# Kernel optimization log

Hardware: AMD Instinct MI355X
Metric: run time of the kernel (lower is better)

## Reference

```python
import jax, jax.numpy as jnp
import numpy as np

T, B, IN, H, OUT = 128, 128, 512, 512, 512


def _lstm_dir(x, W_ih, W_hh, b_ih, b_hh):
    # x: [T, B, IN]; W_ih: [4H, IN]; W_hh: [4H, H]; biases: [4H]
    # Precompute input contribution for all timesteps in one big GEMM.
    xw = jnp.einsum('tbi,gi->tbg', x, W_ih) + b_ih + b_hh  # [T, B, 4H]
    Hh = W_hh.shape[1]

    def step(carry, xw_t):
        h, c = carry
        gates = xw_t + h @ W_hh.T  # [B, 4H]
        i, f, g, o = jnp.split(gates, 4, axis=-1)  # PyTorch gate order i,f,g,o
        i = jax.nn.sigmoid(i)
        f = jax.nn.sigmoid(f)
        g = jnp.tanh(g)
        o = jax.nn.sigmoid(o)
        c = f * c + i * g
        h = o * jnp.tanh(c)
        return (h, c), h

    h0 = jnp.zeros((x.shape[1], Hh), x.dtype)
    c0 = jnp.zeros((x.shape[1], Hh), x.dtype)
    _, hs = jax.lax.scan(step, (h0, c0), xw)
    return hs  # [T, B, H]


def setup_inputs() -> dict:
    key = jax.random.key(0)
    ks = jax.random.split(key, 12)
    s_in = 1.0 / np.sqrt(H)
    u = lambda k, shape: jax.random.uniform(k, shape, jnp.float32, -s_in, s_in)
    return {
        'x': jax.random.normal(ks[0], (T, B, IN), jnp.float32),
        'W_ih_f': u(ks[1], (4 * H, IN)),
        'W_hh_f': u(ks[2], (4 * H, H)),
        'b_ih_f': u(ks[3], (4 * H,)),
        'b_hh_f': u(ks[4], (4 * H,)),
        'W_ih_b': u(ks[5], (4 * H, IN)),
        'W_hh_b': u(ks[6], (4 * H, H)),
        'b_ih_b': u(ks[7], (4 * H,)),
        'b_hh_b': u(ks[8], (4 * H,)),
        'W_lin': u(ks[9], (OUT, 2 * H)),
        'b_lin': u(ks[10], (OUT,)),
    }


def reference(x, W_ih_f, W_hh_f, b_ih_f, b_hh_f, W_ih_b, W_hh_b, b_ih_b, b_hh_b, W_lin, b_lin):
    h_fwd = _lstm_dir(x, W_ih_f, W_hh_f, b_ih_f, b_hh_f)                    # [T,B,H]
    h_bwd = _lstm_dir(x[::-1], W_ih_b, W_hh_b, b_ih_b, b_hh_b)[::-1]        # [T,B,H]
    out = jnp.concatenate([h_fwd, h_bwd], axis=-1)                          # [T,B,2H]
    out = jnp.einsum('tbh,oh->tbo', out, W_lin) + b_lin                     # [T,B,OUT]
    return out
```

## Files before the change

### kernel.cpp

```cpp
#include <hip/hip_runtime.h>

typedef unsigned short u16;
typedef unsigned long long u64;
typedef __attribute__((ext_vector_type(8))) short bf16x8;
typedef __attribute__((ext_vector_type(4))) float f32x4;

#define MFMA16(a, b, c) __builtin_amdgcn_mfma_f32_16x16x32_bf16((a), (b), (c), 0, 0, 0)

#define TT 128
#define BB 128
#define IN_ 512
#define HH 512
#define G4 2048
#define OUTD 512
#define TB 16384

__device__ __forceinline__ u16 f2bf(float f) {
    union { float f; unsigned u; } v; v.f = f;
    unsigned r = v.u + 0x7FFFu + ((v.u >> 16) & 1u);
    return (u16)(r >> 16);
}
__device__ __forceinline__ float bf2f(u16 h) {
    union { unsigned u; float f; } v; v.u = ((unsigned)h) << 16; return v.f;
}
__device__ __forceinline__ float sigmoid_f(float x) { return 1.f / (1.f + __expf(-x)); }
__device__ __forceinline__ float tanh_f(float x) {
    float e = __expf(2.f * x);
    return 1.f - 2.f / (e + 1.f);
}

__global__ void cvt_kernel(const float* __restrict__ src, u16* __restrict__ dst, int n4) {
    int i = blockIdx.x * blockDim.x + threadIdx.x;
    int stride = gridDim.x * blockDim.x;
    for (; i < n4; i += stride) {
        float4 v = ((const float4*)src)[i];
        ushort4 o;
        o.x = f2bf(v.x); o.y = f2bf(v.y); o.z = f2bf(v.z); o.w = f2bf(v.w);
        ((ushort4*)dst)[i] = o;
    }
}

__global__ void bias_kernel(const float* __restrict__ bihf, const float* __restrict__ bhhf,
                            float* __restrict__ bf_, const float* __restrict__ bihb,
                            const float* __restrict__ bhhb, float* __restrict__ bb_, int n) {
    int i = blockIdx.x * blockDim.x + threadIdx.x;
    if (i < n) {
        bf_[i] = bihf[i] + bhhf[i];
        bb_[i] = bihb[i] + bhhb[i];
    }
}

__global__ void zero_exch_kernel(uint4* __restrict__ p) {
    int i = blockIdx.x * blockDim.x + threadIdx.x;
    p[i] = uint4{0u, 0u, 0u, 0u};
}

__global__ __launch_bounds__(256) void gemm_bias_kernel(
    const u16* __restrict__ A, const u16* __restrict__ W,
    const float* __restrict__ bias, void* __restrict__ Cout,
    int M, int N, int K, int out_is_bf16) {
    __shared__ __align__(16) u16 lA[128 * 72];
    __shared__ __align__(16) u16 lB[128 * 72];
    const int tid = threadIdx.x;
    const int m0 = blockIdx.x * 128;
    const int n0 = blockIdx.y * 128;
    const int wave = tid >> 6, lane = tid & 63;
    const int wm = wave >> 1, wn = wave & 1;
    const int lrow = lane & 15, lq = lane >> 4;

    f32x4 acc[4][4] = {};

    for (int kc = 0; kc < K; kc += 64) {
        #pragma unroll
        for (int i = 0; i < 4; ++i) {
            int c = i * 256 + tid;
            int row = c >> 3, off = c & 7;
            *(uint4*)(&lA[row * 72 + off * 8]) =
                *(const uint4*)(&A[(size_t)(m0 + row) * K + kc + off * 8]);
            *(uint4*)(&lB[row * 72 + off * 8]) =
                *(const uint4*)(&W[(size_t)(n0 + row) * K + kc + off * 8]);
        }
        __syncthreads();
        #pragma unroll
        for (int ks = 0; ks < 2; ++ks) {
            bf16x8 af[4], bfr[4];
            #pragma unroll
            for (int mf = 0; mf < 4; ++mf)
                af[mf] = *(const bf16x8*)(&lA[(wm * 64 + mf * 16 + lrow) * 72 + ks * 32 + lq * 8]);
            #pragma unroll
            for (int nf = 0; nf < 4; ++nf)
                bfr[nf] = *(const bf16x8*)(&lB[(wn * 64 + nf * 16 + lrow) * 72 + ks * 32 + lq * 8]);
            #pragma unroll
            for (int mf = 0; mf < 4; ++mf)
                #pragma unroll
                for (int nf = 0; nf < 4; ++nf)
                    acc[mf][nf] = MFMA16(af[mf], bfr[nf], acc[mf][nf]);
        }
        __syncthreads();
    }

    #pragma unroll
    for (int mf = 0; mf < 4; ++mf) {
        #pragma unroll
        for (int nf = 0; nf < 4; ++nf) {
            int row = m0 + wm * 64 + mf * 16 + lq * 4;
            int col = n0 + wn * 64 + nf * 16 + lrow;
            float bv = bias[col];
            f32x4 v = acc[mf][nf];
            #pragma unroll
            for (int r = 0; r < 4; ++r) {
                float val = v[r] + bv;
                if (out_is_bf16)
                    ((u16*)Cout)[(size_t)(row + r) * N + col] = f2bf(val);
                else
                    ((float*)Cout)[(size_t)(row + r) * N + col] = val;
            }
        }
    }
}

__global__ __launch_bounds__(256, 1) void lstm_persist_kernel(
    const u16* __restrict__ xw_f, const u16* __restrict__ xw_b,
    const u16* __restrict__ whh_f, const u16* __restrict__ whh_b,
    u16* __restrict__ hcat, u64* __restrict__ exch) {
    const int bx = blockIdx.x;
    const int dir = bx >> 7;
    const int bt = (bx >> 4) & 7;
    const int jt = bx & 15;
    const u16* __restrict__ xw  = dir ? xw_b : xw_f;
    const u16* __restrict__ whh = dir ? whh_b : whh_f;
    const int b0 = bt * 16;
    const int j0 = jt * 32;

    __shared__ __align__(16) u16 lh[16 * 520];
    __shared__ float sgate[4][16][33];

    const int tid = threadIdx.x;
    const int wave = tid >> 6, lane = tid & 63;
    const int lrow = lane & 15, lq = lane >> 4;

    const u16* wrow = whh + ((size_t)wave * HH + j0) * HH;
    bf16x8 w0[16], w1[16];
    #pragma unroll
    for (int kc = 0; kc < 16; ++kc) {
        w0[kc] = *(const bf16x8*)(&wrow[(size_t)lrow * HH + kc * 32 + lq * 8]);
        w1[kc] = *(const bf16x8*)(&wrow[(size_t)(16 + lrow) * HH + kc * 32 + lq * 8]);
    }
    #pragma unroll
    for (int kc = 0; kc < 16; ++kc)
        asm volatile("" : "+v"(w0[kc]), "+v"(w1[kc]));

    const int bl = tid >> 4;
    const int jj = (tid & 15) * 2;
    float cr0 = 0.f, cr1 = 0.f;

    const size_t my_ex = ((size_t)(dir)*BB + b0 + bl) * 256 + (j0 >> 1) + (tid & 15);

    for (int s = 0; s < TT; ++s) {
        const int t = dir ? (TT - 1 - s) : s;

        const u16* xrow = xw + ((size_t)t * BB + b0 + bl) * G4 + j0 + jj;
        unsigned xg[4];
        #pragma unroll
        for (int g = 0; g < 4; ++g)
            xg[g] = *(const unsigned*)(xrow + (size_t)g * HH);

        f32x4 acc0 = {}, acc1 = {}, acc0b = {}, acc1b = {};
        if (s > 0) {
            const int p = (s - 1) & 1;
            const u64* ex = exch + ((size_t)(p * 2 + dir) * BB + b0) * 256 + tid;
            const u64 expect = ((u64)(unsigned)s << 48) | ((u64)(unsigned)s << 16);
            u64 v[16];
            for (;;) {
                #pragma unroll
                for (int i = 0; i < 16; ++i)
                    v[i] = __hip_atomic_load(ex + (size_t)i * 256,
                                             __ATOMIC_RELAXED, __HIP_MEMORY_SCOPE_AGENT);
                bool ok = true;
                #pragma unroll
                for (int i = 0; i < 16; ++i)
                    ok &= ((v[i] & 0xFFFF0000FFFF0000ull) == expect);
                if (ok) break;
            }
            #pragma unroll
            for (int i = 0; i < 16; ++i)
                *(unsigned*)(&lh[i * 520 + tid * 2]) =
                    (unsigned)(v[i] & 0xffffu) | (unsigned)((v[i] >> 16) & 0xffff0000u);
            __syncthreads();

            #pragma unroll
            for (int kc = 0; kc < 16; kc += 2) {
                bf16x8 a0 = *(const bf16x8*)(&lh[lrow * 520 + kc * 32 + lq * 8]);
                bf16x8 a1 = *(const bf16x8*)(&lh[lrow * 520 + (kc + 1) * 32 + lq * 8]);
                acc0  = MFMA16(a0, w0[kc], acc0);
                acc1  = MFMA16(a0, w1[kc], acc1);
                acc0b = MFMA16(a1, w0[kc + 1], acc0b);
                acc1b = MFMA16(a1, w1[kc + 1], acc1b);
            }
            acc0 += acc0b;
            acc1 += acc1b;
        }

        #pragma unroll
        for (int r = 0; r < 4; ++r) {
            sgate[wave][lq * 4 + r][lrow]      = acc0[r];
            sgate[wave][lq * 4 + r][16 + lrow] = acc1[r];
        }
        __syncthreads();

        float gi0 = sgate[0][bl][jj]     + bf2f((u16)(xg[0] & 0xffffu));
        float gf0 = sgate[1][bl][jj]     + bf2f((u16)(xg[1] & 0xffffu));
        float gg0 = sgate[2][bl][jj]     + bf2f((u16)(xg[2] & 0xffffu));
        float go0 = sgate[3][bl][jj]     + bf2f((u16)(xg[3] & 0xffffu));
        float gi1 = sgate[0][bl][jj + 1] + bf2f((u16)(xg[0] >> 16));
        float gf1 = sgate[1][bl][jj + 1] + bf2f((u16)(xg[1] >> 16));
        float gg1 = sgate[2][bl][jj + 1] + bf2f((u16)(xg[2] >> 16));
        float go1 = sgate[3][bl][jj + 1] + bf2f((u16)(xg[3] >> 16));

        float c0 = sigmoid_f(gf0) * cr0 + sigmoid_f(gi0) * tanh_f(gg0);
        float c1 = sigmoid_f(gf1) * cr1 + sigmoid_f(gi1) * tanh_f(gg1);
        cr0 = c0; cr1 = c1;
        float h0 = sigmoid_f(go0) * tanh_f(c0);
        float h1 = sigmoid_f(go1) * tanh_f(c1);

        unsigned hb0 = (unsigned)f2bf(h0), hb1 = (unsigned)f2bf(h1);
        unsigned tagv = (unsigned)(s + 1) << 16;
        u64 pv = (u64)(tagv | hb0) | ((u64)(tagv | hb1) << 32);
        __hip_atomic_store(exch + (size_t)((s & 1) * 2) * BB * 256 + my_ex, pv,
                           __ATOMIC_RELAXED, __HIP_MEMORY_SCOPE_AGENT);

        *(unsigned*)(hcat + ((size_t)t * BB + b0 + bl) * (2 * HH) + dir * HH + j0 + jj) =
            hb0 | (hb1 << 16);
    }
}

#define OFF_XBF    ((size_t)0)
#define OFF_WIHF   (OFF_XBF  + (size_t)TB * IN_ * 2)
#define OFF_WIHB   (OFF_WIHF + (size_t)G4 * IN_ * 2)
#define OFF_WHHF   (OFF_WIHB + (size_t)G4 * IN_ * 2)
#define OFF_WHHB   (OFF_WHHF + (size_t)G4 * HH * 2)
#define OFF_WLIN   (OFF_WHHB + (size_t)G4 * HH * 2)
#define OFF_BIASF  (OFF_WLIN + (size_t)OUTD * 2 * HH * 2)
#define OFF_BIASB  (OFF_BIASF + (size_t)G4 * 4)
#define OFF_XWF    (OFF_BIASB + (size_t)G4 * 4)
#define OFF_XWB    (OFF_XWF  + (size_t)TB * G4 * 2)
#define OFF_HCAT   (OFF_XWB  + (size_t)TB * G4 * 2)
#define OFF_EXCH   (OFF_HCAT + (size_t)TB * 2 * HH * 2)
#define WS_NEED    (OFF_EXCH + (size_t)2 * 2 * BB * HH * 4)

extern "C" void kernel_launch(void* const* d_in, const int* in_sizes, int n_in,
                              void* d_out, int out_size, void* d_ws, size_t ws_size,
                              hipStream_t stream) {
    (void)in_sizes; (void)n_in; (void)out_size;
    if (ws_size < WS_NEED) return;

    const float* x    = (const float*)d_in[0];
    const float* Wihf = (const float*)d_in[1];
    const float* Whhf = (const float*)d_in[2];
    const float* bihf = (const float*)d_in[3];
    const float* bhhf = (const float*)d_in[4];
    const float* Wihb = (const float*)d_in[5];
    const float* Whhb = (const float*)d_in[6];
    const float* bihb = (const float*)d_in[7];
    const float* bhhb = (const float*)d_in[8];
    const float* Wlin = (const float*)d_in[9];
    const float* blin = (const float*)d_in[10];
    float* out = (float*)d_out;

    char* ws = (char*)d_ws;
    u16* x_bf    = (u16*)(ws + OFF_XBF);
    u16* wihf_bf = (u16*)(ws + OFF_WIHF);
    u16* wihb_bf = (u16*)(ws + OFF_WIHB);
    u16* whhf_bf = (u16*)(ws + OFF_WHHF);
    u16* whhb_bf = (u16*)(ws + OFF_WHHB);
    u16* wlin_bf = (u16*)(ws + OFF_WLIN);
    float* bias_f = (float*)(ws + OFF_BIASF);
    float* bias_b = (float*)(ws + OFF_BIASB);
    u16* xw_f = (u16*)(ws + OFF_XWF);
    u16* xw_b = (u16*)(ws + OFF_XWB);
    u16* hcat = (u16*)(ws + OFF_HCAT);
    u64* exch = (u64*)(ws + OFF_EXCH);

    cvt_kernel<<<2048, 256, 0, stream>>>(x, x_bf, (TB * IN_) / 4);
    cvt_kernel<<<512, 256, 0, stream>>>(Wihf, wihf_bf, (G4 * IN_) / 4);
    cvt_kernel<<<512, 256, 0, stream>>>(Wihb, wihb_bf, (G4 * IN_) / 4);
    cvt_kernel<<<512, 256, 0, stream>>>(Whhf, whhf_bf, (G4 * HH) / 4);
    cvt_kernel<<<512, 256, 0, stream>>>(Whhb, whhb_bf, (G4 * HH) / 4);
    cvt_kernel<<<512, 256, 0, stream>>>(Wlin, wlin_bf, (OUTD * 2 * HH) / 4);
    bias_kernel<<<8, 256, 0, stream>>>(bihf, bhhf, bias_f, bihb, bhhb, bias_b, G4);
    zero_exch_kernel<<<256, 256, 0, stream>>>((uint4*)exch);

    gemm_bias_kernel<<<dim3(TB / 128, G4 / 128), 256, 0, stream>>>(
        x_bf, wihf_bf, bias_f, xw_f, TB, G4, IN_, 1);
    gemm_bias_kernel<<<dim3(TB / 128, G4 / 128), 256, 0, stream>>>(
        x_bf, wihb_bf, bias_b, xw_b, TB, G4, IN_, 1);

    {
        void* args[] = { (void*)&xw_f, (void*)&xw_b, (void*)&whhf_bf, (void*)&whhb_bf,
                         (void*)&hcat, (void*)&exch };
        hipError_t e = hipLaunchCooperativeKernel(
            (const void*)lstm_persist_kernel, dim3(256), dim3(256), args, 0, stream);
        if (e != hipSuccess) {
            lstm_persist_kernel<<<256, 256, 0, stream>>>(xw_f, xw_b, whhf_bf, whhb_bf,
                                                         hcat, exch);
        }
    }

    gemm_bias_kernel<<<dim3(TB / 128, OUTD / 128), 256, 0, stream>>>(
        hcat, wlin_bf, blin, out, TB, OUTD, 2 * HH, 0);
}
```

Baseline: 698.1 us.

## Split recurrent GEMM over K across waves and feed MFMA directly from exchange loads

Each wave now owns a quarter of the hidden-state K dimension for all four gates, rather than one gate over the full K. Each lane loads its MFMA A-operand straight from the global exchange buffer, polls per chunk and strips tags in registers. This removes the LDS staging of h and one barrier, and lets MFMAs start on chunks that have already arrived. In exchange it needs a cross-wave reduction of partial sums through a larger shared buffer, and it adds an extra barrier before that buffer is written.

```diff
diff --git a/kernel.cpp b/kernel.cpp
--- a/kernel.cpp
+++ b/kernel.cpp
@@ -15,6 +15,8 @@
 #define OUTD 512
 #define TB 16384
 
+#define AEXLD(p) __hip_atomic_load((p), __ATOMIC_RELAXED, __HIP_MEMORY_SCOPE_AGENT)
+
 __device__ __forceinline__ u16 f2bf(float f) {
     union { float f; unsigned u; } v; v.f = f;
     unsigned r = v.u + 0x7FFFu + ((v.u >> 16) & 1u);
@@ -27,6 +29,9 @@
 __device__ __forceinline__ float tanh_f(float x) {
     float e = __expf(2.f * x);
     return 1.f - 2.f / (e + 1.f);
+}
+__device__ __forceinline__ unsigned striptag(u64 v) {
+    return (unsigned)(v & 0xffffu) | ((unsigned)(v >> 16) & 0xffff0000u);
 }
 
 __global__ void cvt_kernel(const float* __restrict__ src, u16* __restrict__ dst, int n4) {
@@ -132,29 +137,39 @@
     const int b0 = bt * 16;
     const int j0 = jt * 32;
 
-    __shared__ __align__(16) u16 lh[16 * 520];
-    __shared__ float sgate[4][16][33];
+    __shared__ float sg[4][4][16][33];
 
     const int tid = threadIdx.x;
     const int wave = tid >> 6, lane = tid & 63;
     const int lrow = lane & 15, lq = lane >> 4;
 
-    const u16* wrow = whh + ((size_t)wave * HH + j0) * HH;
-    bf16x8 w0[16], w1[16];
+    bf16x8 wreg[4][2][4];
     #pragma unroll
-    for (int kc = 0; kc < 16; ++kc) {
-        w0[kc] = *(const bf16x8*)(&wrow[(size_t)lrow * HH + kc * 32 + lq * 8]);
-        w1[kc] = *(const bf16x8*)(&wrow[(size_t)(16 + lrow) * HH + kc * 32 + lq * 8]);
-    }
+    for (int g = 0; g < 4; ++g)
+        #pragma unroll
+        for (int jh = 0; jh < 2; ++jh)
+            #pragma unroll
+            for (int ci = 0; ci < 4; ++ci)
+                wreg[g][jh][ci] = *(const bf16x8*)
+                    (&whh[(size_t)(g * HH + j0 + jh * 16 + lrow) * HH +
+                          (wave + ci * 4) * 32 + lq * 8]);
     #pragma unroll
-    for (int kc = 0; kc < 16; ++kc)
-        asm volatile("" : "+v"(w0[kc]), "+v"(w1[kc]));
+    for (int g = 0; g < 4; ++g)
+        #pragma unroll
+        for (int jh = 0; jh < 2; ++jh)
+            #pragma unroll
+            for (int ci = 0; ci < 4; ++ci)
+                asm volatile("" : "+v"(wreg[g][jh][ci]));
 
     const int bl = tid >> 4;
     const int jj = (tid & 15) * 2;
     float cr0 = 0.f, cr1 = 0.f;
 
-    const size_t my_ex = ((size_t)(dir)*BB + b0 + bl) * 256 + (j0 >> 1) + (tid & 15);
+    const size_t my_ex = ((size_t)dir * BB + b0 + bl) * 256 + (j0 >> 1) + (tid & 15);
+    const u64* exb0 = exch + ((size_t)(0 * 2 + dir) * BB + b0 + lrow) * 256 + lq * 4;
+    const u64* exb1 = exch + ((size_t)(1 * 2 + dir) * BB + b0 + lrow) * 256 + lq * 4;
+
+    const u64 TMASK = 0xFFFF0000FFFF0000ull;
 
     for (int s = 0; s < TT; ++s) {
         const int t = dir ? (TT - 1 - s) : s;
@@ -165,63 +180,70 @@
         for (int g = 0; g < 4; ++g)
             xg[g] = *(const unsigned*)(xrow + (size_t)g * HH);
 
-        f32x4 acc0 = {}, acc1 = {}, acc0b = {}, acc1b = {};
+        f32x4 acc[4][2] = {};
         if (s > 0) {
-            const int p = (s - 1) & 1;
-            const u64* ex = exch + ((size_t)(p * 2 + dir) * BB + b0) * 256 + tid;
+            const u64* eb = ((s - 1) & 1) ? exb1 : exb0;
             const u64 expect = ((u64)(unsigned)s << 48) | ((u64)(unsigned)s << 16);
-            u64 v[16];
-            for (;;) {
-                #pragma unroll
-                for (int i = 0; i < 16; ++i)
-                    v[i] = __hip_atomic_load(ex + (size_t)i * 256,
-                                             __ATOMIC_RELAXED, __HIP_MEMORY_SCOPE_AGENT);
-                bool ok = true;
-                #pragma unroll
-                for (int i = 0; i < 16; ++i)
-                    ok &= ((v[i] & 0xFFFF0000FFFF0000ull) == expect);
-                if (ok) break;
+
+            u64 v[4][4];
+            #pragma unroll
+            for (int ci = 0; ci < 4; ++ci) {
+                const u64* cp = eb + (size_t)(wave + ci * 4) * 16;
+                #pragma unroll
+                for (int k = 0; k < 4; ++k)
+                    v[ci][k] = AEXLD(cp + k);
             }
             #pragma unroll
-            for (int i = 0; i < 16; ++i)
-                *(unsigned*)(&lh[i * 520 + tid * 2]) =
-                    (unsigned)(v[i] & 0xffffu) | (unsigned)((v[i] >> 16) & 0xffff0000u);
-            __syncthreads();
-
-            #pragma unroll
-            for (int kc = 0; kc < 16; kc += 2) {
-                bf16x8 a0 = *(const bf16x8*)(&lh[lrow * 520 + kc * 32 + lq * 8]);
-                bf16x8 a1 = *(const bf16x8*)(&lh[lrow * 520 + (kc + 1) * 32 + lq * 8]);
-                acc0  = MFMA16(a0, w0[kc], acc0);
-                acc1  = MFMA16(a0, w1[kc], acc1);
-                acc0b = MFMA16(a1, w0[kc + 1], acc0b);
-                acc1b = MFMA16(a1, w1[kc + 1], acc1b);
+            for (int ci = 0; ci < 4; ++ci) {
+                const u64* cp = eb + (size_t)(wave + ci * 4) * 16;
+                for (;;) {
+                    bool ok = ((v[ci][0] & TMASK) == expect) &
+                              ((v[ci][1] & TMASK) == expect) &
+                              ((v[ci][2] & TMASK) == expect) &
+                              ((v[ci][3] & TMASK) == expect);
+                    if (ok) break;
+                    #pragma unroll
+                    for (int k = 0; k < 4; ++k)
+                        v[ci][k] = AEXLD(cp + k);
+                }
+                union { unsigned u[4]; bf16x8 b8; } ua;
+                #pragma unroll
+                for (int k = 0; k < 4; ++k)
+                    ua.u[k] = striptag(v[ci][k]);
+                bf16x8 a = ua.b8;
+                #pragma unroll
+                for (int g = 0; g < 4; ++g) {
+                    acc[g][0] = MFMA16(a, wreg[g][0][ci], acc[g][0]);
+                    acc[g][1] = MFMA16(a, wreg[g][1][ci], acc[g][1]);
+                }
             }
-            acc0 += acc0b;
-            acc1 += acc1b;
-        }
-
-        #pragma unroll
-        for (int r = 0; r < 4; ++r) {
-            sgate[wave][lq * 4 + r][lrow]      = acc0[r];
-            sgate[wave][lq * 4 + r][16 + lrow] = acc1[r];
-        }
+        }
+
         __syncthreads();
-
-        float gi0 = sgate[0][bl][jj]     + bf2f((u16)(xg[0] & 0xffffu));
-        float gf0 = sgate[1][bl][jj]     + bf2f((u16)(xg[1] & 0xffffu));
-        float gg0 = sgate[2][bl][jj]     + bf2f((u16)(xg[2] & 0xffffu));
-        float go0 = sgate[3][bl][jj]     + bf2f((u16)(xg[3] & 0xffffu));
-        float gi1 = sgate[0][bl][jj + 1] + bf2f((u16)(xg[0] >> 16));
-        float gf1 = sgate[1][bl][jj + 1] + bf2f((u16)(xg[1] >> 16));
-        float gg1 = sgate[2][bl][jj + 1] + bf2f((u16)(xg[2] >> 16));
-        float go1 = sgate[3][bl][jj + 1] + bf2f((u16)(xg[3] >> 16));
-
-        float c0 = sigmoid_f(gf0) * cr0 + sigmoid_f(gi0) * tanh_f(gg0);
-        float c1 = sigmoid_f(gf1) * cr1 + sigmoid_f(gi1) * tanh_f(gg1);
+        #pragma unroll
+        for (int g = 0; g < 4; ++g)
+            #pragma unroll
+            for (int jh = 0; jh < 2; ++jh)
+                #pragma unroll
+                for (int r = 0; r < 4; ++r)
+                    sg[wave][g][lq * 4 + r][jh * 16 + lrow] = acc[g][jh][r];
+        __syncthreads();
+
+        float gv0[4], gv1[4];
+        #pragma unroll
+        for (int g = 0; g < 4; ++g) {
+            gv0[g] = sg[0][g][bl][jj] + sg[1][g][bl][jj] +
+                     sg[2][g][bl][jj] + sg[3][g][bl][jj] +
+                     bf2f((u16)(xg[g] & 0xffffu));
+            gv1[g] = sg[0][g][bl][jj + 1] + sg[1][g][bl][jj + 1] +
+                     sg[2][g][bl][jj + 1] + sg[3][g][bl][jj + 1] +
+                     bf2f((u16)(xg[g] >> 16));
+        }
+        float c0 = sigmoid_f(gv0[1]) * cr0 + sigmoid_f(gv0[0]) * tanh_f(gv0[2]);
+        float c1 = sigmoid_f(gv1[1]) * cr1 + sigmoid_f(gv1[0]) * tanh_f(gv1[2]);
         cr0 = c0; cr1 = c1;
-        float h0 = sigmoid_f(go0) * tanh_f(c0);
-        float h1 = sigmoid_f(go1) * tanh_f(c1);
+        float h0 = sigmoid_f(gv0[3]) * tanh_f(c0);
+        float h1 = sigmoid_f(gv1[3]) * tanh_f(c1);
 
         unsigned hb0 = (unsigned)f2bf(h0), hb1 = (unsigned)f2bf(h1);
         unsigned tagv = (unsigned)(s + 1) << 16;
```

After: 859.3 us. 1.23x slower.
